# Performance work log

Hardware: AMD Instinct MI355X
Metric: run time of the kernel (lower is better)

## Reference

```python
import jax, jax.numpy as jnp
import numpy as np

H, KV, D = 16, 4, 128
EPS = 1e-6

def setup_inputs() -> dict:
    key = jax.random.key(0)
    ks = jax.random.split(key, 7)
    B, S, HS = 2, 2048, 2048
    return {
        "hidden_states": jax.random.normal(ks[0], (B, S, HS), jnp.float32),
        "cos": jax.random.uniform(ks[1], (S, D), jnp.float32),
        "sin": jax.random.uniform(ks[2], (S, D), jnp.float32),
        "Wq": jax.random.normal(ks[3], (H * D, HS), jnp.float32) * 0.02,
        "Wk": jax.random.normal(ks[4], (KV * D, HS), jnp.float32) * 0.02,
        "Wv": jax.random.normal(ks[5], (KV * D, HS), jnp.float32) * 0.02,
        "Wo": jax.random.normal(ks[6], (HS, H * D), jnp.float32) * 0.02,
        "norm_q_w": jnp.ones((D,), jnp.float32),
        "norm_k_w": jnp.ones((D,), jnp.float32),
    }

def _rmsnorm(x, w):
    # RMSNorm over head_dim
    return x * jax.lax.rsqrt(jnp.mean(x * x, axis=-1, keepdims=True) + EPS) * w

def _rope(x, cos, sin):
    # x: [B, S, heads, D]; cos/sin: [S, D]; rotate-half (use_real_unbind_dim=-2)
    c = cos[None, :, None, :]
    s = sin[None, :, None, :]
    x1, x2 = jnp.split(x, 2, axis=-1)
    x_rot = jnp.concatenate([-x2, x1], axis=-1)
    return x * c + x_rot * s

def reference(hidden_states, cos, sin, Wq, Wk, Wv, Wo, norm_q_w, norm_k_w):
    B, S, _ = hidden_states.shape
    q = (hidden_states @ Wq.T).reshape(B, S, H, D)
    k = (hidden_states @ Wk.T).reshape(B, S, KV, D)
    v = (hidden_states @ Wv.T).reshape(B, S, KV, D)
    q = _rmsnorm(q, norm_q_w)
    k = _rmsnorm(k, norm_k_w)
    q = _rope(q, cos, sin)
    k = _rope(k, cos, sin)
    # GQA: repeat_interleave K/V heads to match Q heads
    g = H // KV
    k = jnp.repeat(k, g, axis=2)  # [B, S, H, D]
    v = jnp.repeat(v, g, axis=2)
    scores = jnp.einsum('bqhd,bkhd->bhqk', q, k) * (D ** -0.5)
    attn = jax.nn.softmax(scores, axis=-1)
    out = jnp.einsum('bhqk,bkhd->bqhd', attn, v)  # [B, S, H, D]
    out = out.reshape(B, S, H * D)
    return out @ Wo.T
```

## Files before the change

### kernel.cpp

```cpp
#include <hip/hip_runtime.h>


typedef __attribute__((ext_vector_type(8))) short bf16x8;
typedef __attribute__((ext_vector_type(4))) float f32x4;
typedef __attribute__((ext_vector_type(16))) float f32x16;

__device__ __forceinline__ unsigned short f2bf(float x) {
  union { float f; unsigned u; } v; v.f = x;
  unsigned r = v.u + 0x7fffu + ((v.u >> 16) & 1u);
  return (unsigned short)(r >> 16);
}

__device__ __forceinline__ float bf2f(unsigned short h) {
  union { unsigned u; float f; } v; v.u = (unsigned)h << 16;
  return v.f;
}

__device__ __forceinline__ unsigned cvt_pk_bf16(float lo, float hi) {
  unsigned r;
  asm("v_cvt_pk_bf16_f32 %0, %1, %2" : "=v"(r) : "v"(lo), "v"(hi));
  return r;
}

__device__ __forceinline__ void gload_lds16(const void* g, void* l) {
  __builtin_amdgcn_global_load_lds(
      (const __attribute__((address_space(1))) void*)g,
      (__attribute__((address_space(3))) void*)l, 16, 0, 0);
}

__global__ __launch_bounds__(256) void cvt4(const float4* __restrict__ in,
                                            ushort4* __restrict__ out, int n4) {
  int i = blockIdx.x * 256 + threadIdx.x;
  if (i < n4) {
    float4 v = in[i];
    out[i] = make_ushort4(f2bf(v.x), f2bf(v.y), f2bf(v.z), f2bf(v.w));
  }
}

template <int NF, bool OUT_BF16>
__global__ __launch_bounds__(512, 2) void gemm_bt_8ph(
    const unsigned short* __restrict__ A, const unsigned short* __restrict__ Bm,
    void* __restrict__ Cout, int M, int N, int K) {
  __shared__ char lsA[2][32768];
  __shared__ char lsB[2][NF * 8192];
  const int tid = threadIdx.x;
  const int wave = tid >> 6, lane = tid & 63;
  const int lrow = lane & 15, kg = lane >> 4;
  const int wm = wave >> 2, wn = wave & 3;
  const int BN = NF * 64;
  const int nbn = N / BN;
  const int bid = (blockIdx.x & 7) * (gridDim.x >> 3) + (blockIdx.x >> 3);
  const int m0 = (bid / nbn) << 8;
  const int n0 = (bid % nbn) * BN;
  const int NT = K >> 6;

  const int srow = tid >> 2;
  const int scol = (((tid & 3) ^ (srow & 3)) << 3);
  const size_t a0 = (size_t)(m0 + srow) * K + scol;
  const size_t a1 = (size_t)(m0 + 128 + srow) * K + scol;
  const size_t b0 = (size_t)(n0 + srow) * K + scol;
  const size_t b1 = (size_t)(n0 + 128 + srow) * K + scol;

  f32x4 acc[8][NF];
#pragma unroll
  for (int i = 0; i < 8; ++i)
#pragma unroll
    for (int j = 0; j < NF; ++j)
#pragma unroll
      for (int t = 0; t < 4; ++t) acc[i][j][t] = 0.f;

  const int xk = ((kg ^ (lrow & 3)) << 4);
  const int abase = (wm * 128 + lrow) * 64 + xk;
  const int bbase = (wn * NF * 16 + lrow) * 64 + xk;

  auto stage_plane = [&](int T, int ks) {
    if (T >= NT) return;
    const int buf = T & 1;
    const size_t kof = (size_t)T * 64 + ks * 32;
    char* da = lsA[buf] + ks * 16384 + wave * 1024;
    gload_lds16(A + a0 + kof, da);
    gload_lds16(A + a1 + kof, da + 8192);
    char* db = lsB[buf] + ks * (NF * 4096) + wave * 1024;
    gload_lds16(Bm + b0 + kof, db);
    if (NF >= 3) {
      if (tid < 256) gload_lds16(Bm + b1 + kof, db + 8192);
    }
  };

  auto phase = [&](int T, int ks, int sT, int sKs) {
    const int buf = T & 1;
    const char* pa = lsA[buf] + ks * 16384;
    const char* pb = lsB[buf] + ks * (NF * 4096);
    bf16x8 af[8], bfr[NF];
#pragma unroll
    for (int mf = 0; mf < 8; ++mf)
      af[mf] = *(const bf16x8*)(pa + abase + mf * 1024);
#pragma unroll
    for (int nf = 0; nf < NF; ++nf)
      bfr[nf] = *(const bf16x8*)(pb + bbase + nf * 1024);
    stage_plane(sT, sKs);
    asm volatile("s_waitcnt vmcnt(6)" ::: "memory");
    __builtin_amdgcn_s_barrier();
    asm volatile("s_waitcnt lgkmcnt(0)" ::: "memory");
    __builtin_amdgcn_sched_barrier(0);
    __builtin_amdgcn_s_setprio(1);
#pragma unroll
    for (int mf = 0; mf < 8; ++mf)
#pragma unroll
      for (int nf = 0; nf < NF; ++nf)
        acc[mf][nf] =
            __builtin_amdgcn_mfma_f32_16x16x32_bf16(af[mf], bfr[nf], acc[mf][nf], 0, 0, 0);
    __builtin_amdgcn_s_setprio(0);
    __builtin_amdgcn_s_barrier();
  };

  stage_plane(0, 0);
  stage_plane(0, 1);
  stage_plane(1, 0);
  asm volatile("s_waitcnt vmcnt(6)" ::: "memory");
  __builtin_amdgcn_s_barrier();

  for (int kt = 0; kt < NT; ++kt) {
    phase(kt, 0, kt + 1, 1);
    phase(kt, 1, kt + 2, 0);
  }

#pragma unroll
  for (int mf = 0; mf < 8; ++mf) {
#pragma unroll
    for (int nf = 0; nf < NF; ++nf) {
      int row = m0 + wm * 128 + mf * 16 + kg * 4;
      int col = n0 + wn * NF * 16 + nf * 16 + lrow;
      if (OUT_BF16) {
        unsigned short* C = (unsigned short*)Cout;
#pragma unroll
        for (int t = 0; t < 4; ++t)
          C[(size_t)(row + t) * N + col] = f2bf(acc[mf][nf][t]);
      } else {
        float* C = (float*)Cout;
#pragma unroll
        for (int t = 0; t < 4; ++t)
          C[(size_t)(row + t) * N + col] = acc[mf][nf][t];
      }
    }
  }
}

__global__ __launch_bounds__(256) void rms_rope(
    const unsigned short* __restrict__ QKV, const float* __restrict__ cosT,
    const float* __restrict__ sinT, const float* __restrict__ wq,
    const float* __restrict__ wk, unsigned short* __restrict__ Q,
    unsigned short* __restrict__ Kg, unsigned short* __restrict__ Vg) {
  int task = blockIdx.x * 4 + (threadIdx.x >> 6);
  int lane = threadIdx.x & 63;
  int row = task / 24;
  int slot = task - row * 24;
  int b = row >> 11, s = row & 2047;
  const unsigned short* x = QKV + (size_t)row * 3072 + slot * 128;
  float x1 = bf2f(x[lane]), x2 = bf2f(x[lane + 64]);
  if (slot < 20) {
    float ss = x1 * x1 + x2 * x2;
#pragma unroll
    for (int msk = 1; msk < 64; msk <<= 1) ss += __shfl_xor(ss, msk);
    float inv = rsqrtf(ss * (1.0f / 128.0f) + 1e-6f);
    const float* w = (slot < 16) ? wq : wk;
    x1 *= inv * w[lane];
    x2 *= inv * w[lane + 64];
    float c1 = cosT[s * 128 + lane], c2 = cosT[s * 128 + lane + 64];
    float sn1 = sinT[s * 128 + lane], sn2 = sinT[s * 128 + lane + 64];
    float o1 = x1 * c1 - x2 * sn1;
    float o2 = x2 * c2 + x1 * sn2;
    if (slot < 16) {
      const float qs = 0.08838834764831845f * 1.4426950408889634f;
      o1 *= qs; o2 *= qs;
    }
    x1 = o1; x2 = o2;
  }
  if (slot < 16) {
    unsigned short* dst = Q + (((size_t)b * 16 + slot) * 2048 + s) * 128;
    dst[lane] = f2bf(x1);
    dst[lane + 64] = f2bf(x2);
  } else {
    int kv = (slot - 16) & 3;
    size_t tb = ((size_t)((b * 4 + kv) * 32) + (s >> 6)) * 16384;
    int key = s & 63;
    if (slot < 20) {
      char* base = (char*)Kg + tb;
      int kb = (key >> 5) * 512 + (key & 31) * 16;
      int d1 = lane, d2 = lane + 64;
      *(unsigned short*)(base + (d1 >> 4) * 2048 + ((d1 >> 3) & 1) * 1024 + kb + (d1 & 7) * 2) = f2bf(x1);
      *(unsigned short*)(base + (d2 >> 4) * 2048 + ((d2 >> 3) & 1) * 1024 + kb + (d2 & 7) * 2) = f2bf(x2);
    } else {
      char* base = (char*)Vg + tb;
      int p = key >> 4;
      int vhi = (key >> 2) & 1;
      int e = (key & 3) | (((key >> 3) & 1) << 2);
      int off = p * 4096 + vhi * 512 + e * 2;
      int d1 = lane, d2 = lane + 64;
      *(unsigned short*)(base + off + (d1 >> 5) * 1024 + (d1 & 31) * 16) = f2bf(x1);
      *(unsigned short*)(base + off + (d2 >> 5) * 1024 + (d2 & 31) * 16) = f2bf(x2);
    }
  }
}

__global__ __launch_bounds__(256, 2) void attn64(
    const unsigned short* __restrict__ Q, const unsigned short* __restrict__ Kg,
    const unsigned short* __restrict__ Vg, unsigned short* __restrict__ O) {
  __shared__ unsigned short Kl[2][8192];
  const int tid = threadIdx.x;
  const int wave = tid >> 6, lane = tid & 63;
  const int l31 = lane & 31, hi = lane >> 5;
  int bid = blockIdx.x;
  bid = (bid & 7) * 64 + (bid >> 3);
  const int bh = bid >> 4, qt = bid & 15;
  const int b = bh >> 4, h = bh & 15, kh = h >> 2;
  const char* Kt = (const char*)Kg + (size_t)(b * 4 + kh) * 524288;
  const char* Vt = (const char*)Vg + (size_t)(b * 4 + kh) * 524288;
  const unsigned short* Qb =
      Q + ((size_t)(b * 16 + h) * 2048 + qt * 128 + wave * 32) * 128;
  bf16x8 qf[8];
#pragma unroll
  for (int s = 0; s < 8; ++s)
    qf[s] = *(const bf16x8*)(Qb + l31 * 128 + s * 16 + hi * 8);
  f32x16 acc[4];
#pragma unroll
  for (int c = 0; c < 4; ++c)
#pragma unroll
    for (int r = 0; r < 16; ++r) acc[c][r] = 0.f;
  float lsum = 0.f;

  const char* Vlane = Vt + hi * 512 + l31 * 16;
  bf16x8 vr[16];

  auto stageK = [&](int t) {
    const char* kt = Kt + (size_t)t * 16384;
    char* kd = (char*)Kl[t & 1];
#pragma unroll
    for (int c = 0; c < 4; ++c)
      gload_lds16(kt + c * 4096 + tid * 16, kd + c * 4096 + wave * 1024);
  };
  auto loadV = [&](int t) {
    const char* vt = Vlane + (size_t)t * 16384;
#pragma unroll
    for (int p = 0; p < 4; ++p)
#pragma unroll
      for (int c = 0; c < 4; ++c)
        vr[p * 4 + c] = *(const bf16x8*)(vt + p * 4096 + c * 1024);
  };

  loadV(0);
  stageK(0);
  asm volatile("s_waitcnt vmcnt(0)" ::: "memory");
  __builtin_amdgcn_s_barrier();

  f32x16 s0, s1;
  for (int t = 0; t < 32; ++t) {
    if (t < 31) stageK(t + 1);
    {
      const char* Kb = (const char*)Kl[t & 1] + hi * 1024 + l31 * 16;
#pragma unroll
      for (int r = 0; r < 16; ++r) { s0[r] = 0.f; s1[r] = 0.f; }
      __builtin_amdgcn_s_setprio(1);
#pragma unroll
      for (int s = 0; s < 8; ++s) {
        bf16x8 k0 = *(const bf16x8*)(Kb + s * 2048);
        bf16x8 k1 = *(const bf16x8*)(Kb + s * 2048 + 512);
        s0 = __builtin_amdgcn_mfma_f32_32x32x16_bf16(k0, qf[s], s0, 0, 0, 0);
        s1 = __builtin_amdgcn_mfma_f32_32x32x16_bf16(k1, qf[s], s1, 0, 0, 0);
      }
      __builtin_amdgcn_s_setprio(0);
    }
    float p0[16], p1[16];
#pragma unroll
    for (int r = 0; r < 16; ++r) {
      p0[r] = exp2f(s0[r]);
      p1[r] = exp2f(s1[r]);
    }
    float u8[8];
#pragma unroll
    for (int r = 0; r < 8; ++r) u8[r] = (p0[r] + p0[r + 8]) + (p1[r] + p1[r + 8]);
#pragma unroll
    for (int r = 0; r < 4; ++r) u8[r] += u8[r + 4];
    lsum += (u8[0] + u8[1]) + (u8[2] + u8[3]);
    union { bf16x8 v[4]; unsigned w[16]; } pa;
#pragma unroll
    for (int r = 0; r < 4; ++r) {
      pa.w[r]      = cvt_pk_bf16(p0[2 * r], p0[2 * r + 1]);
      pa.w[4 + r]  = cvt_pk_bf16(p0[8 + 2 * r], p0[9 + 2 * r]);
      pa.w[8 + r]  = cvt_pk_bf16(p1[2 * r], p1[2 * r + 1]);
      pa.w[12 + r] = cvt_pk_bf16(p1[8 + 2 * r], p1[9 + 2 * r]);
    }
    __builtin_amdgcn_s_setprio(1);
#pragma unroll
    for (int p = 0; p < 4; ++p)
#pragma unroll
      for (int c = 0; c < 4; ++c)
        acc[c] = __builtin_amdgcn_mfma_f32_32x32x16_bf16(pa.v[p], vr[p * 4 + c], acc[c], 0, 0, 0);
    __builtin_amdgcn_s_setprio(0);
    if (t < 31) {
      loadV(t + 1);
      asm volatile("s_waitcnt vmcnt(16)" ::: "memory");
      __builtin_amdgcn_s_barrier();
    }
  }

  lsum += __shfl_xor(lsum, 32);
  float inv = 1.0f / lsum;
#pragma unroll
  for (int r = 0; r < 16; ++r) {
    int q = (r & 3) + 8 * (r >> 2) + 4 * hi;
    float invq = __shfl(inv, q);
    int srow = qt * 128 + wave * 32 + q;
    unsigned short* dst = O + (((size_t)b * 2048 + srow) * 16 + h) * 128;
#pragma unroll
    for (int c = 0; c < 4; ++c)
      dst[c * 32 + l31] = f2bf(acc[c][r] * invq);
  }
}

extern "C" void kernel_launch(void* const* d_in, const int* in_sizes, int n_in,
                              void* d_out, int out_size, void* d_ws, size_t ws_size,
                              hipStream_t stream) {
  const float* hs   = (const float*)d_in[0];
  const float* cosT = (const float*)d_in[1];
  const float* sinT = (const float*)d_in[2];
  const float* Wq   = (const float*)d_in[3];
  const float* Wk   = (const float*)d_in[4];
  const float* Wv   = (const float*)d_in[5];
  const float* Wo   = (const float*)d_in[6];
  const float* nqw  = (const float*)d_in[7];
  const float* nkw  = (const float*)d_in[8];
  float* out = (float*)d_out;

  char* ws = (char*)d_ws;
  unsigned short* X    = (unsigned short*)ws;
  unsigned short* Wqkv = X + 8388608;
  unsigned short* WoB  = Wqkv + 6291456;
  unsigned short* QKVb = WoB + 4194304;
  unsigned short* Qb   = QKVb + 12582912;
  unsigned short* Kg   = Qb + 8388608;
  unsigned short* Vg   = Kg + 2097152;
  unsigned short* Ob   = QKVb;

  cvt4<<<8192, 256, 0, stream>>>((const float4*)hs, (ushort4*)X, 2097152);
  cvt4<<<4096, 256, 0, stream>>>((const float4*)Wq, (ushort4*)Wqkv, 1048576);
  cvt4<<<1024, 256, 0, stream>>>((const float4*)Wk, (ushort4*)(Wqkv + 4194304), 262144);
  cvt4<<<1024, 256, 0, stream>>>((const float4*)Wv, (ushort4*)(Wqkv + 5242880), 262144);
  cvt4<<<4096, 256, 0, stream>>>((const float4*)Wo, (ushort4*)WoB, 1048576);

  gemm_bt_8ph<3, true><<<256, 512, 0, stream>>>(X, Wqkv, QKVb, 4096, 3072, 2048);

  rms_rope<<<24576, 256, 0, stream>>>(QKVb, cosT, sinT, nqw, nkw, Qb, Kg, Vg);

  attn64<<<512, 256, 0, stream>>>(Qb, Kg, Vg, Ob);

  gemm_bt_8ph<2, false><<<256, 512, 0, stream>>>(Ob, WoB, out, 4096, 2048, 2048);
}
```

Measured before the change: 235.6 us.

## Split attention over two KV halves with separate combine kernel

Attention now splits the key range into two halves, doubling the grid to 1024 blocks. Each block writes unnormalized fp32 partial outputs and row sums, and a new combine kernel adds the two halves, normalizes and converts to bf16. Launch bounds are raised to request higher occupancy. This targets underfilled CUs with only 512 blocks, at the cost of extra fp32 partial traffic (about 64MB written and read) and one more launch. Correctness depends on the softmax using no running max, so the partial sums combine directly.

```diff
diff --git a/kernel.cpp b/kernel.cpp
--- a/kernel.cpp
+++ b/kernel.cpp
@@ -203,19 +203,20 @@
   }
 }
 
-__global__ __launch_bounds__(256, 2) void attn64(
+__global__ __launch_bounds__(256, 4) void attn64(
     const unsigned short* __restrict__ Q, const unsigned short* __restrict__ Kg,
-    const unsigned short* __restrict__ Vg, unsigned short* __restrict__ O) {
+    const unsigned short* __restrict__ Vg, float* __restrict__ P0,
+    float* __restrict__ P1, float* __restrict__ Ls) {
   __shared__ unsigned short Kl[2][8192];
   const int tid = threadIdx.x;
   const int wave = tid >> 6, lane = tid & 63;
   const int l31 = lane & 31, hi = lane >> 5;
   int bid = blockIdx.x;
-  bid = (bid & 7) * 64 + (bid >> 3);
-  const int bh = bid >> 4, qt = bid & 15;
+  bid = (bid & 7) * 128 + (bid >> 3);
+  const int qt = bid & 15, sp = (bid >> 4) & 1, bh = bid >> 5;
   const int b = bh >> 4, h = bh & 15, kh = h >> 2;
-  const char* Kt = (const char*)Kg + (size_t)(b * 4 + kh) * 524288;
-  const char* Vt = (const char*)Vg + (size_t)(b * 4 + kh) * 524288;
+  const char* Kt = (const char*)Kg + (size_t)(b * 4 + kh) * 524288 + (size_t)sp * 262144;
+  const char* Vt = (const char*)Vg + (size_t)(b * 4 + kh) * 524288 + (size_t)sp * 262144;
   const unsigned short* Qb =
       Q + ((size_t)(b * 16 + h) * 2048 + qt * 128 + wave * 32) * 128;
   bf16x8 qf[8];
@@ -254,8 +255,8 @@
   __builtin_amdgcn_s_barrier();
 
   f32x16 s0, s1;
-  for (int t = 0; t < 32; ++t) {
-    if (t < 31) stageK(t + 1);
+  for (int t = 0; t < 16; ++t) {
+    if (t < 15) stageK(t + 1);
     {
       const char* Kb = (const char*)Kl[t & 1] + hi * 1024 + l31 * 16;
 #pragma unroll
@@ -297,7 +298,7 @@
       for (int c = 0; c < 4; ++c)
         acc[c] = __builtin_amdgcn_mfma_f32_32x32x16_bf16(pa.v[p], vr[p * 4 + c], acc[c], 0, 0, 0);
     __builtin_amdgcn_s_setprio(0);
-    if (t < 31) {
+    if (t < 15) {
       loadV(t + 1);
       asm volatile("s_waitcnt vmcnt(16)" ::: "memory");
       __builtin_amdgcn_s_barrier();
@@ -305,17 +306,41 @@
   }
 
   lsum += __shfl_xor(lsum, 32);
-  float inv = 1.0f / lsum;
+  float* Pp = sp ? P1 : P0;
+  if (hi == 0) {
+    int srow = qt * 128 + wave * 32 + l31;
+    Ls[(size_t)sp * 65536 + ((size_t)b * 2048 + srow) * 16 + h] = lsum;
+  }
 #pragma unroll
   for (int r = 0; r < 16; ++r) {
     int q = (r & 3) + 8 * (r >> 2) + 4 * hi;
-    float invq = __shfl(inv, q);
     int srow = qt * 128 + wave * 32 + q;
-    unsigned short* dst = O + (((size_t)b * 2048 + srow) * 16 + h) * 128;
+    float* dst = Pp + (((size_t)b * 2048 + srow) * 16 + h) * 128;
 #pragma unroll
     for (int c = 0; c < 4; ++c)
-      dst[c * 32 + l31] = f2bf(acc[c][r] * invq);
-  }
+      dst[c * 32 + l31] = acc[c][r];
+  }
+}
+
+__global__ __launch_bounds__(256) void attn_combine(
+    const float* __restrict__ P0, const float* __restrict__ P1,
+    const float* __restrict__ Ls, unsigned short* __restrict__ Ob) {
+  int gid = blockIdx.x * 256 + threadIdx.x;
+  int row = gid >> 4, c = gid & 15;
+  float inv = 1.0f / (Ls[row] + Ls[65536 + row]);
+  const float4* a = (const float4*)(P0 + (size_t)row * 128 + c * 8);
+  const float4* bb = (const float4*)(P1 + (size_t)row * 128 + c * 8);
+  float4 a0 = a[0], a1 = a[1], b0 = bb[0], b1 = bb[1];
+  union { bf16x8 v; unsigned short u[8]; } o;
+  o.u[0] = f2bf((a0.x + b0.x) * inv);
+  o.u[1] = f2bf((a0.y + b0.y) * inv);
+  o.u[2] = f2bf((a0.z + b0.z) * inv);
+  o.u[3] = f2bf((a0.w + b0.w) * inv);
+  o.u[4] = f2bf((a1.x + b1.x) * inv);
+  o.u[5] = f2bf((a1.y + b1.y) * inv);
+  o.u[6] = f2bf((a1.z + b1.z) * inv);
+  o.u[7] = f2bf((a1.w + b1.w) * inv);
+  *(bf16x8*)(Ob + (size_t)row * 128 + c * 8) = o.v;
 }
 
 extern "C" void kernel_launch(void* const* d_in, const int* in_sizes, int n_in,
@@ -333,14 +358,17 @@
   float* out = (float*)d_out;
 
   char* ws = (char*)d_ws;
-  unsigned short* X    = (unsigned short*)ws;
-  unsigned short* Wqkv = X + 8388608;
-  unsigned short* WoB  = Wqkv + 6291456;
-  unsigned short* QKVb = WoB + 4194304;
-  unsigned short* Qb   = QKVb + 12582912;
+  unsigned short* WoB  = (unsigned short*)ws;
+  unsigned short* Qb   = WoB + 4194304;
   unsigned short* Kg   = Qb + 8388608;
   unsigned short* Vg   = Kg + 2097152;
-  unsigned short* Ob   = QKVb;
+  unsigned short* X    = Vg + 2097152;
+  unsigned short* Wqkv = X + 8388608;
+  unsigned short* QKVb = Wqkv + 6291456;
+  float* P0            = (float*)X;
+  float* P1            = P0 + 8388608;
+  float* Ls            = P1 + 8388608;
+  unsigned short* Ob   = Qb;
 
   cvt4<<<8192, 256, 0, stream>>>((const float4*)hs, (ushort4*)X, 2097152);
   cvt4<<<4096, 256, 0, stream>>>((const float4*)Wq, (ushort4*)Wqkv, 1048576);
@@ -352,7 +380,9 @@
 
   rms_rope<<<24576, 256, 0, stream>>>(QKVb, cosT, sinT, nqw, nkw, Qb, Kg, Vg);
 
-  attn64<<<512, 256, 0, stream>>>(Qb, Kg, Vg, Ob);
+  attn64<<<1024, 256, 0, stream>>>(Qb, Kg, Vg, P0, P1, Ls);
+
+  attn_combine<<<4096, 256, 0, stream>>>(P0, P1, Ls, Ob);
 
   gemm_bt_8ph<2, false><<<256, 512, 0, stream>>>(Ob, WoB, out, 4096, 2048, 2048);
 }
```

New measurement: 720.5 us. +205.8%, slower.
